# Kernel optimization log

Hardware: AMD Instinct MI355X
Metric: run time of the kernel (lower is better)

Reference implementation:

```python
import jax, jax.numpy as jnp
import numpy as np

N_NODES = 50000
N_EDGES = 800000
F_IN = 128
HIDDEN = 256
N_GRAPHS = 128


def setup_inputs() -> dict:
    key = jax.random.key(0)
    ks = jax.random.split(key, 13)
    x = jax.random.normal(ks[0], (N_NODES, F_IN), dtype=jnp.float32)
    edge_src = jax.random.randint(ks[1], (N_EDGES,), 0, N_NODES, dtype=jnp.int32)
    edge_dst = jax.random.randint(ks[2], (N_EDGES,), 0, N_NODES, dtype=jnp.int32)
    edge_w = jax.random.uniform(ks[3], (N_EDGES,), dtype=jnp.float32)
    seg_ids = jnp.sort(jax.random.randint(ks[4], (N_NODES,), 0, N_GRAPHS, dtype=jnp.int32))
    def lin(k, fan_in, fan_out):
        s = 1.0 / np.sqrt(fan_in)
        return jax.random.uniform(k, (fan_in, fan_out), dtype=jnp.float32, minval=-s, maxval=s)
    W1 = lin(ks[5], F_IN, HIDDEN);  b1 = jnp.zeros((HIDDEN,), jnp.float32)
    W2 = lin(ks[6], HIDDEN, HIDDEN); b2 = jnp.zeros((HIDDEN,), jnp.float32)
    Wd = lin(ks[7], HIDDEN, HIDDEN); bd = jnp.zeros((HIDDEN,), jnp.float32)
    Wo = lin(ks[8], HIDDEN, 1);      bo = jnp.zeros((1,), jnp.float32)
    return {"x": x, "edge_src": edge_src, "edge_dst": edge_dst, "edge_w": edge_w,
            "seg_ids": seg_ids, "W1": W1, "b1": b1, "W2": W2, "b2": b2,
            "Wd": Wd, "bd": bd, "Wo": Wo, "bo": bo}


def reference(x, edge_src, edge_dst, edge_w, seg_ids, W1, b1, W2, b2, Wd, bd, Wo, bo):
    n_nodes = x.shape[0]

    def spmm(h):
        # sparse A_norm @ h via gather-scale-scatter over the edge list
        msg = h[edge_src] * edge_w[:, None]            # [E, H]
        return jax.ops.segment_sum(msg, edge_dst, num_segments=n_nodes)

    # GCNConv 1: relu(A @ X @ W1 + b1); dropout p=0 is identity
    h = jax.nn.relu(spmm(x @ W1) + b1)                 # [N, H]
    # GCNConv 2
    h = jax.nn.relu(spmm(h @ W2) + b2)                 # [N, H]
    # GlobalSumPool keyed by graph index
    g = jax.ops.segment_sum(h, seg_ids, num_segments=N_GRAPHS)  # [G, H]
    # dense head
    g = jax.nn.relu(g @ Wd + bd)
    return g @ Wo + bo                                 # [G, 1]
```

## Files before the change

### kernel.cpp

```cpp
#include <hip/hip_runtime.h>
#include <hip/hip_bf16.h>


typedef short v8s __attribute__((ext_vector_type(8)));
typedef float v4f __attribute__((ext_vector_type(4)));
typedef float v2f __attribute__((ext_vector_type(2)));

#define BKT_CAP 6144

__device__ inline unsigned bf16u(float f) {
    unsigned u = __builtin_bit_cast(unsigned, f);
    return (u + 0x7fffu + ((u >> 16) & 1u)) >> 16;
}
__device__ inline float bflo(unsigned v) { return __builtin_bit_cast(float, v << 16); }
__device__ inline float bfhi(unsigned v) { return __builtin_bit_cast(float, v & 0xffff0000u); }

__global__ __launch_bounds__(256) void prep(
    const float* __restrict__ x, unsigned char* __restrict__ x8,
    const float* __restrict__ W1, ushort* __restrict__ Wt1,
    const float* __restrict__ W2, ushort* __restrict__ Wt2,
    int* __restrict__ bcnt)
{
    int b = blockIdx.x;
    int t = threadIdx.x;
    if (b < 6250) {
        int i = b * 256 + t;
        if (i < 1600000) {
            float4 v = ((const float4*)x)[i];
            int pk = __builtin_amdgcn_cvt_pk_fp8_f32(v.x, v.y, 0, false);
            pk = __builtin_amdgcn_cvt_pk_fp8_f32(v.z, v.w, pk, true);
            ((unsigned*)x8)[i] = (unsigned)pk;
        }
    } else if (b < 6506) {
        int n = b - 6250;
        if (t < 128) Wt1[n * 128 + t] = (ushort)bf16u(W1[t * 256 + n]);
    } else if (b < 6762) {
        int n = b - 6506;
        Wt2[n * 256 + t] = (ushort)bf16u(W2[t * 256 + n]);
    } else {
        bcnt[t] = 0;
    }
}

__global__ __launch_bounds__(256) void bin_pass(
    const int* __restrict__ src, const int* __restrict__ dst,
    const float* __restrict__ w, int* __restrict__ bcnt,
    uint2* __restrict__ stage, float* __restrict__ g, int E)
{
    __shared__ int hist[256];
    __shared__ int excl[256];
    __shared__ int gbase[256];
    __shared__ uint2 stg[2048];

    int t = threadIdx.x, b = blockIdx.x;
    if (b < 128) g[b * 256 + t] = 0.f;

    int e0 = b * 2048;
    hist[t] = 0;
    __syncthreads();

    int d_[8]; unsigned pk_[8]; int rk_[8]; int bk_[8];
    #pragma unroll
    for (int j = 0; j < 8; j++) {
        int e = e0 + t + j * 256;
        if (e < E) {
            int d = dst[e];
            d_[j] = d;
            bk_[j] = d >> 8;
            pk_[j] = (unsigned)src[e] | (bf16u(w[e]) << 16);
            rk_[j] = atomicAdd(&hist[bk_[j]], 1);
        } else d_[j] = -1;
    }
    __syncthreads();

    int cnt = hist[t];
    excl[t] = cnt;
    __syncthreads();
    for (int o = 1; o < 256; o <<= 1) {
        int v = (t >= o) ? excl[t - o] : 0;
        __syncthreads();
        excl[t] += v;
        __syncthreads();
    }
    int ex = excl[t] - cnt;
    if (cnt > 0) gbase[t] = atomicAdd(&bcnt[t], cnt);
    __syncthreads();
    excl[t] = ex;
    __syncthreads();

    #pragma unroll
    for (int j = 0; j < 8; j++)
        if (d_[j] >= 0)
            stg[excl[bk_[j]] + rk_[j]] = make_uint2(pk_[j], (unsigned)d_[j]);
    __syncthreads();

    int nval = min(2048, E - e0);
    #pragma unroll
    for (int j = 0; j < 8; j++) {
        int sidx = t + j * 256;
        if (sidx < nval) {
            uint2 ent = stg[sidx];
            int bk = (int)(ent.y >> 8);
            stage[(size_t)bk * BKT_CAP + gbase[bk] + sidx - excl[bk]] = ent;
        }
    }
}

__global__ __launch_bounds__(256) void sort_build(
    const uint2* __restrict__ stage, const int* __restrict__ bcnt,
    unsigned* __restrict__ edges, int* __restrict__ off, int N, int E)
{
    __shared__ unsigned sorted[BKT_CAP];
    __shared__ int hist[256];
    __shared__ int s[256];
    __shared__ int cur[256];
    __shared__ int psum[4];
    __shared__ int sbase;

    int t = threadIdx.x, b = blockIdx.x;
    const uint2* reg = stage + (size_t)b * BKT_CAP;
    int cnt = bcnt[b];

    int pred = (t < b) ? bcnt[t] : 0;
    #pragma unroll
    for (int o = 32; o > 0; o >>= 1) pred += __shfl_down(pred, o, 64);
    if ((t & 63) == 0) psum[t >> 6] = pred;
    hist[t] = 0;
    __syncthreads();
    if (t == 0) sbase = psum[0] + psum[1] + psum[2] + psum[3];

    for (int i = t; i < cnt; i += 256)
        atomicAdd(&hist[reg[i].y & 255u], 1);
    __syncthreads();

    int h = hist[t];
    s[t] = h;
    __syncthreads();
    for (int o = 1; o < 256; o <<= 1) {
        int v = (t >= o) ? s[t - o] : 0;
        __syncthreads();
        s[t] += v;
        __syncthreads();
    }
    int ex = s[t] - h;
    cur[t] = ex;
    __syncthreads();

    int nn = b * 256 + t;
    if (nn <= N) off[nn] = sbase + ex;

    for (int i = t; i < cnt; i += 256) {
        uint2 ent = reg[i];
        int r = atomicAdd(&cur[ent.y & 255u], 1);
        sorted[r] = ent.x;
    }
    __syncthreads();
    for (int i = t; i < cnt; i += 256)
        edges[sbase + i] = sorted[i];
}

__global__ __launch_bounds__(256) void spmm128(
    const unsigned char* __restrict__ x8, const int* __restrict__ off,
    const unsigned* __restrict__ edges, ushort* __restrict__ S, int n)
{
    int node = blockIdx.x * 4 + (threadIdx.x >> 6);
    if (node >= n) return;
    int lane = threadIdx.x & 63;
    const ushort* base = (const ushort*)x8;
    int e0 = off[node], e1 = off[node + 1];
    float a0 = 0.f, a1 = 0.f;
    int e = e0;
    for (; e + 16 <= e1; e += 16) {
        unsigned ed[16]; ushort v[16];
        #pragma unroll
        for (int j = 0; j < 16; j++) ed[j] = edges[e + j];
        #pragma unroll
        for (int j = 0; j < 16; j++)
            v[j] = base[(size_t)(ed[j] & 0xffffu) * 64 + lane];
        #pragma unroll
        for (int j = 0; j < 16; j++) {
            float w = bfhi(ed[j]);
            v2f f = __builtin_amdgcn_cvt_pk_f32_fp8((int)v[j], false);
            a0 += f.x * w;
            a1 += f.y * w;
        }
    }
    for (; e + 4 <= e1; e += 4) {
        unsigned ed[4]; ushort v[4];
        #pragma unroll
        for (int j = 0; j < 4; j++) ed[j] = edges[e + j];
        #pragma unroll
        for (int j = 0; j < 4; j++)
            v[j] = base[(size_t)(ed[j] & 0xffffu) * 64 + lane];
        #pragma unroll
        for (int j = 0; j < 4; j++) {
            float w = bfhi(ed[j]);
            v2f f = __builtin_amdgcn_cvt_pk_f32_fp8((int)v[j], false);
            a0 += f.x * w;
            a1 += f.y * w;
        }
    }
    for (; e < e1; e++) {
        unsigned ed = edges[e];
        float w0 = bfhi(ed);
        ushort v0 = base[(size_t)(ed & 0xffffu) * 64 + lane];
        v2f f0 = __builtin_amdgcn_cvt_pk_f32_fp8((int)v0, false);
        a0 += f0.x * w0;
        a1 += f0.y * w0;
    }
    ((unsigned*)S)[(size_t)node * 64 + lane] = (bf16u(a1) << 16) | bf16u(a0);
}

__global__ __launch_bounds__(256) void spmm256(
    const unsigned char* __restrict__ h8, const int* __restrict__ off,
    const unsigned* __restrict__ edges, ushort* __restrict__ S, int n)
{
    int node = blockIdx.x * 4 + (threadIdx.x >> 6);
    if (node >= n) return;
    int lane = threadIdx.x & 63;
    const unsigned* base = (const unsigned*)h8;
    int e0 = off[node], e1 = off[node + 1];
    float a0 = 0.f, a1 = 0.f, a2 = 0.f, a3 = 0.f;
    int e = e0;
    for (; e + 16 <= e1; e += 16) {
        unsigned ed[16]; unsigned v[16];
        #pragma unroll
        for (int j = 0; j < 16; j++) ed[j] = edges[e + j];
        #pragma unroll
        for (int j = 0; j < 16; j++)
            v[j] = base[(size_t)(ed[j] & 0xffffu) * 64 + lane];
        #pragma unroll
        for (int j = 0; j < 16; j++) {
            float w = bfhi(ed[j]);
            v2f l = __builtin_amdgcn_cvt_pk_f32_fp8((int)v[j], false);
            v2f h = __builtin_amdgcn_cvt_pk_f32_fp8((int)v[j], true);
            a0 += l.x * w;
            a1 += l.y * w;
            a2 += h.x * w;
            a3 += h.y * w;
        }
    }
    for (; e + 4 <= e1; e += 4) {
        unsigned ed[4]; unsigned v[4];
        #pragma unroll
        for (int j = 0; j < 4; j++) ed[j] = edges[e + j];
        #pragma unroll
        for (int j = 0; j < 4; j++)
            v[j] = base[(size_t)(ed[j] & 0xffffu) * 64 + lane];
        #pragma unroll
        for (int j = 0; j < 4; j++) {
            float w = bfhi(ed[j]);
            v2f l = __builtin_amdgcn_cvt_pk_f32_fp8((int)v[j], false);
            v2f h = __builtin_amdgcn_cvt_pk_f32_fp8((int)v[j], true);
            a0 += l.x * w;
            a1 += l.y * w;
            a2 += h.x * w;
            a3 += h.y * w;
        }
    }
    for (; e < e1; e++) {
        unsigned ed = edges[e];
        float w0 = bfhi(ed);
        unsigned v0 = base[(size_t)(ed & 0xffffu) * 64 + lane];
        v2f l0 = __builtin_amdgcn_cvt_pk_f32_fp8((int)v0, false);
        v2f h0 = __builtin_amdgcn_cvt_pk_f32_fp8((int)v0, true);
        a0 += l0.x * w0;
        a1 += l0.y * w0;
        a2 += h0.x * w0;
        a3 += h0.y * w0;
    }
    uint2 o;
    o.x = (bf16u(a1) << 16) | bf16u(a0);
    o.y = (bf16u(a3) << 16) | bf16u(a2);
    ((uint2*)S)[(size_t)node * 64 + lane] = o;
}

template <int K, int OFMT, bool POOL>
__global__ __launch_bounds__(512) void gemm_tile(
    const ushort* __restrict__ A, const ushort* __restrict__ Wt,
    const float* __restrict__ bias, void* __restrict__ out,
    const int* __restrict__ seg, float* __restrict__ g, int M)
{
    __shared__ __align__(16) ushort As[128 * 32];
    __shared__ __align__(16) ushort Bs[256 * 32];
    __shared__ int segsh[128];

    const int tid = threadIdx.x;
    const int bm = blockIdx.x * 128;
    const int wave = tid >> 6, lane = tid & 63;
    const int wm = wave >> 2, wn = wave & 3;
    const int r = lane & 15, q = lane >> 4;

    if (POOL && tid < 128) {
        int gr = bm + tid;
        segsh[tid] = (gr < M) ? seg[gr] : 0x7fffffff;
    }

    const int o0 = tid * 16;
    const int row0 = o0 >> 6;
    const int kb0 = o0 & 63;

    const char* Ab = (const char*)A;
    const char* Bb = (const char*)Wt;

    uint4 ra0, rb0, rb1;
    ra0 = *(const uint4*)(Ab + ((size_t)(bm + row0) * K) * 2 + kb0);
    rb0 = *(const uint4*)(Bb + ((size_t)(row0)       * K) * 2 + kb0);
    rb1 = *(const uint4*)(Bb + ((size_t)(row0 + 128) * K) * 2 + kb0);

    v4f acc[4][4];
    #pragma unroll
    for (int i = 0; i < 4; i++)
        #pragma unroll
        for (int j = 0; j < 4; j++) acc[i][j] = (v4f){0.f, 0.f, 0.f, 0.f};

    const int NK = K / 32;
    for (int ks = 0; ks < NK; ks++) {
        __syncthreads();
        *(uint4*)((char*)As + o0)        = ra0;
        *(uint4*)((char*)Bs + o0)        = rb0;
        *(uint4*)((char*)Bs + o0 + 8192) = rb1;
        if (ks + 1 < NK) {
            const int kof = (ks + 1) * 64;
            ra0 = *(const uint4*)(Ab + ((size_t)(bm + row0) * K) * 2 + kof + kb0);
            rb0 = *(const uint4*)(Bb + ((size_t)(row0)       * K) * 2 + kof + kb0);
            rb1 = *(const uint4*)(Bb + ((size_t)(row0 + 128) * K) * 2 + kof + kb0);
        }
        __syncthreads();

        v8s af[4], bf[4];
        #pragma unroll
        for (int i = 0; i < 4; i++)
            af[i] = *(const v8s*)(As + (wm * 64 + i * 16 + r) * 32 + q * 8);
        #pragma unroll
        for (int j = 0; j < 4; j++)
            bf[j] = *(const v8s*)(Bs + (wn * 64 + j * 16 + r) * 32 + q * 8);
        #pragma unroll
        for (int i = 0; i < 4; i++)
            #pragma unroll
            for (int j = 0; j < 4; j++)
                acc[i][j] = __builtin_amdgcn_mfma_f32_16x16x32_bf16(
                    af[i], bf[j], acc[i][j], 0, 0, 0);
    }

    if constexpr (POOL) {
        #pragma unroll
        for (int j = 0; j < 4; j++) {
            float b = bias[wn * 64 + j * 16 + r];
            #pragma unroll
            for (int i = 0; i < 4; i++)
                #pragma unroll
                for (int ii = 0; ii < 4; ii++)
                    acc[i][j][ii] = fmaxf(acc[i][j][ii] + b, 0.f);
        }
        int myseg[16];
        #pragma unroll
        for (int i = 0; i < 4; i++)
            #pragma unroll
            for (int ii = 0; ii < 4; ii++)
                myseg[i * 4 + ii] = segsh[wm * 64 + i * 16 + q * 4 + ii];
        int s_lo = segsh[0];
        int s_hi = segsh[min(127, M - 1 - bm)];
        for (int s = s_lo; s <= s_hi; s++) {
            #pragma unroll
            for (int j = 0; j < 4; j++) {
                float p = 0.f;
                #pragma unroll
                for (int i = 0; i < 4; i++)
                    #pragma unroll
                    for (int ii = 0; ii < 4; ii++)
                        if (myseg[i * 4 + ii] == s) p += acc[i][j][ii];
                p += __shfl_xor(p, 16, 64);
                p += __shfl_xor(p, 32, 64);
                if (lane < 16)
                    atomicAdd(&g[s * 256 + wn * 64 + j * 16 + r], p);
            }
        }
    } else {
        #pragma unroll
        for (int j = 0; j < 4; j++) {
            int col = wn * 64 + j * 16 + r;
            float b = bias[col];
            #pragma unroll
            for (int i = 0; i < 4; i++) {
                #pragma unroll
                for (int ii = 0; ii < 4; ii++) {
                    int row = bm + wm * 64 + i * 16 + q * 4 + ii;
                    if (row < M) {
                        float v = fmaxf(acc[i][j][ii] + b, 0.f);
                        if constexpr (OFMT == 1) {
                            ((ushort*)out)[(size_t)row * 256 + col] = (ushort)bf16u(v);
                        } else if constexpr (OFMT == 2) {
                            unsigned pk = (unsigned)__builtin_amdgcn_cvt_pk_fp8_f32(
                                v, v, 0, false);
                            ((unsigned char*)out)[(size_t)row * 256 + col] =
                                (unsigned char)(pk & 0xffu);
                        } else {
                            ((float*)out)[(size_t)row * 256 + col] = v;
                        }
                    }
                }
            }
        }
    }
}

__global__ __launch_bounds__(256) void head(
    const float* __restrict__ g, const float* __restrict__ Wd,
    const float* __restrict__ bd, const float* __restrict__ Wo,
    const float* __restrict__ bo, float* __restrict__ out)
{
    __shared__ float gr[256];
    int j = threadIdx.x;
    int gi = blockIdx.x;
    gr[j] = g[(size_t)gi * 256 + j];
    __syncthreads();
    float a2 = bd[j];
    for (int k = 0; k < 256; k++)
        a2 += gr[k] * Wd[(size_t)k * 256 + j];
    a2 = fmaxf(a2, 0.f);

    float v = a2 * Wo[j];
    #pragma unroll
    for (int off = 32; off > 0; off >>= 1)
        v += __shfl_down(v, off, 64);
    __shared__ float partial[4];
    if ((j & 63) == 0) partial[j >> 6] = v;
    __syncthreads();
    if (j == 0)
        out[gi] = partial[0] + partial[1] + partial[2] + partial[3] + bo[0];
}

extern "C" void kernel_launch(void* const* d_in, const int* in_sizes, int n_in,
                              void* d_out, int out_size, void* d_ws, size_t ws_size,
                              hipStream_t stream) {
    const float* x   = (const float*)d_in[0];
    const int*   esrc= (const int*)  d_in[1];
    const int*   edst= (const int*)  d_in[2];
    const float* ew  = (const float*)d_in[3];
    const int*   seg = (const int*)  d_in[4];
    const float* W1  = (const float*)d_in[5];
    const float* b1  = (const float*)d_in[6];
    const float* W2  = (const float*)d_in[7];
    const float* b2  = (const float*)d_in[8];
    const float* Wd  = (const float*)d_in[9];
    const float* bd  = (const float*)d_in[10];
    const float* Wo  = (const float*)d_in[11];
    const float* bo  = (const float*)d_in[12];
    float* out = (float*)d_out;

    const int N = 50000, E = 800000, G = 128, H = 256, F = 128;
    const int NPAD = 50048;
    const int NB = (N + 255) / 256;

    char* p = (char*)d_ws;
    char* region0 = p;                  p += (size_t)N * H * sizeof(float);
    unsigned char* x8 = (unsigned char*)region0;
    ushort* S1 = (ushort*)(region0 + (size_t)N * F);
    uint2* stage = (uint2*)(region0 + (size_t)32 * 1024 * 1024);
    unsigned char* h8 = (unsigned char*)p;
                                        p += (size_t)N * H;
    ushort* S2 = (ushort*)p;            p += (size_t)NPAD * H * sizeof(ushort);
    float* g   = (float*)p;             p += (size_t)G * H * sizeof(float);
    int*   bcnt= (int*)p;               p += 256 * sizeof(int);
    int*   off = (int*)p;               p += (size_t)(N + 1) * sizeof(int) + 12;
    unsigned* edges=(unsigned*)p;       p += (size_t)E * sizeof(unsigned);
    ushort* Wt1= (ushort*)p;            p += (size_t)H * F * sizeof(ushort);
    ushort* Wt2= (ushort*)p;            p += (size_t)H * H * sizeof(ushort);

    prep<<<6763, 256, 0, stream>>>(x, x8, W1, Wt1, W2, Wt2, bcnt);
    bin_pass<<<(E + 2047) / 2048, 256, 0, stream>>>(esrc, edst, ew, bcnt, stage, g, E);
    sort_build<<<NB, 256, 0, stream>>>(stage, bcnt, edges, off, N, E);

    spmm128<<<(N + 3) / 4, 256, 0, stream>>>(x8, off, edges, S1, N);
    gemm_tile<128, 2, false><<<NPAD / 128, 512, 0, stream>>>(
        S1, Wt1, b1, h8, nullptr, nullptr, N);

    spmm256<<<(N + 3) / 4, 256, 0, stream>>>(h8, off, edges, S2, N);
    gemm_tile<256, 0, true><<<NPAD / 128, 512, 0, stream>>>(
        S2, Wt2, b2, nullptr, seg, g, N);

    head<<<G, 256, 0, stream>>>(g, Wd, bd, Wo, bo, out);
}
```

Before: 227.0 us.

## Fuse SpMM aggregation with dense GEMM per 64-node tile in shared memory

Measured after the change: 251.6 us. +10.9%, slower.

```diff
diff --git a/kernel.cpp b/kernel.cpp
--- a/kernel.cpp
+++ b/kernel.cpp
@@ -159,184 +159,167 @@
         edges[sbase + i] = sorted[i];
 }
 
-__global__ __launch_bounds__(256) void spmm128(
-    const unsigned char* __restrict__ x8, const int* __restrict__ off,
-    const unsigned* __restrict__ edges, ushort* __restrict__ S, int n)
-{
-    int node = blockIdx.x * 4 + (threadIdx.x >> 6);
-    if (node >= n) return;
-    int lane = threadIdx.x & 63;
-    const ushort* base = (const ushort*)x8;
-    int e0 = off[node], e1 = off[node + 1];
-    float a0 = 0.f, a1 = 0.f;
-    int e = e0;
-    for (; e + 16 <= e1; e += 16) {
-        unsigned ed[16]; ushort v[16];
-        #pragma unroll
-        for (int j = 0; j < 16; j++) ed[j] = edges[e + j];
-        #pragma unroll
-        for (int j = 0; j < 16; j++)
-            v[j] = base[(size_t)(ed[j] & 0xffffu) * 64 + lane];
-        #pragma unroll
-        for (int j = 0; j < 16; j++) {
-            float w = bfhi(ed[j]);
-            v2f f = __builtin_amdgcn_cvt_pk_f32_fp8((int)v[j], false);
-            a0 += f.x * w;
-            a1 += f.y * w;
-        }
-    }
-    for (; e + 4 <= e1; e += 4) {
-        unsigned ed[4]; ushort v[4];
-        #pragma unroll
-        for (int j = 0; j < 4; j++) ed[j] = edges[e + j];
-        #pragma unroll
-        for (int j = 0; j < 4; j++)
-            v[j] = base[(size_t)(ed[j] & 0xffffu) * 64 + lane];
-        #pragma unroll
-        for (int j = 0; j < 4; j++) {
-            float w = bfhi(ed[j]);
-            v2f f = __builtin_amdgcn_cvt_pk_f32_fp8((int)v[j], false);
-            a0 += f.x * w;
-            a1 += f.y * w;
-        }
-    }
-    for (; e < e1; e++) {
-        unsigned ed = edges[e];
-        float w0 = bfhi(ed);
-        ushort v0 = base[(size_t)(ed & 0xffffu) * 64 + lane];
-        v2f f0 = __builtin_amdgcn_cvt_pk_f32_fp8((int)v0, false);
-        a0 += f0.x * w0;
-        a1 += f0.y * w0;
-    }
-    ((unsigned*)S)[(size_t)node * 64 + lane] = (bf16u(a1) << 16) | bf16u(a0);
-}
-
-__global__ __launch_bounds__(256) void spmm256(
-    const unsigned char* __restrict__ h8, const int* __restrict__ off,
-    const unsigned* __restrict__ edges, ushort* __restrict__ S, int n)
-{
-    int node = blockIdx.x * 4 + (threadIdx.x >> 6);
-    if (node >= n) return;
-    int lane = threadIdx.x & 63;
-    const unsigned* base = (const unsigned*)h8;
-    int e0 = off[node], e1 = off[node + 1];
-    float a0 = 0.f, a1 = 0.f, a2 = 0.f, a3 = 0.f;
-    int e = e0;
-    for (; e + 16 <= e1; e += 16) {
-        unsigned ed[16]; unsigned v[16];
-        #pragma unroll
-        for (int j = 0; j < 16; j++) ed[j] = edges[e + j];
-        #pragma unroll
-        for (int j = 0; j < 16; j++)
-            v[j] = base[(size_t)(ed[j] & 0xffffu) * 64 + lane];
-        #pragma unroll
-        for (int j = 0; j < 16; j++) {
-            float w = bfhi(ed[j]);
-            v2f l = __builtin_amdgcn_cvt_pk_f32_fp8((int)v[j], false);
-            v2f h = __builtin_amdgcn_cvt_pk_f32_fp8((int)v[j], true);
-            a0 += l.x * w;
-            a1 += l.y * w;
-            a2 += h.x * w;
-            a3 += h.y * w;
-        }
-    }
-    for (; e + 4 <= e1; e += 4) {
-        unsigned ed[4]; unsigned v[4];
-        #pragma unroll
-        for (int j = 0; j < 4; j++) ed[j] = edges[e + j];
-        #pragma unroll
-        for (int j = 0; j < 4; j++)
-            v[j] = base[(size_t)(ed[j] & 0xffffu) * 64 + lane];
-        #pragma unroll
-        for (int j = 0; j < 4; j++) {
-            float w = bfhi(ed[j]);
-            v2f l = __builtin_amdgcn_cvt_pk_f32_fp8((int)v[j], false);
-            v2f h = __builtin_amdgcn_cvt_pk_f32_fp8((int)v[j], true);
-            a0 += l.x * w;
-            a1 += l.y * w;
-            a2 += h.x * w;
-            a3 += h.y * w;
-        }
-    }
-    for (; e < e1; e++) {
-        unsigned ed = edges[e];
-        float w0 = bfhi(ed);
-        unsigned v0 = base[(size_t)(ed & 0xffffu) * 64 + lane];
-        v2f l0 = __builtin_amdgcn_cvt_pk_f32_fp8((int)v0, false);
-        v2f h0 = __builtin_amdgcn_cvt_pk_f32_fp8((int)v0, true);
-        a0 += l0.x * w0;
-        a1 += l0.y * w0;
-        a2 += h0.x * w0;
-        a3 += h0.y * w0;
-    }
-    uint2 o;
-    o.x = (bf16u(a1) << 16) | bf16u(a0);
-    o.y = (bf16u(a3) << 16) | bf16u(a2);
-    ((uint2*)S)[(size_t)node * 64 + lane] = o;
-}
-
-template <int K, int OFMT, bool POOL>
-__global__ __launch_bounds__(512) void gemm_tile(
-    const ushort* __restrict__ A, const ushort* __restrict__ Wt,
+template <int KIN, int OFMT, bool POOL>
+__global__ __launch_bounds__(512) void fused_layer(
+    const unsigned char* __restrict__ feat, const int* __restrict__ off,
+    const unsigned* __restrict__ edges, const ushort* __restrict__ Wt,
     const float* __restrict__ bias, void* __restrict__ out,
     const int* __restrict__ seg, float* __restrict__ g, int M)
 {
-    __shared__ __align__(16) ushort As[128 * 32];
+    constexpr int AST = KIN + 8;
+    __shared__ __align__(16) ushort At[64 * AST];
     __shared__ __align__(16) ushort Bs[256 * 32];
-    __shared__ int segsh[128];
+    __shared__ int segsh[64];
 
     const int tid = threadIdx.x;
-    const int bm = blockIdx.x * 128;
+    const int bm = blockIdx.x * 64;
     const int wave = tid >> 6, lane = tid & 63;
+
+    if (POOL && tid < 64) {
+        int gr = bm + tid;
+        segsh[tid] = (gr < M) ? seg[gr] : 0x7fffffff;
+    }
+
+    for (int i = 0; i < 8; i++) {
+        int nl = wave * 8 + i;
+        int node = bm + nl;
+        if (node < M) {
+            int e0 = off[node], e1 = off[node + 1];
+            if (KIN == 256) {
+                const unsigned* base = (const unsigned*)feat;
+                float a0 = 0.f, a1 = 0.f, a2 = 0.f, a3 = 0.f;
+                int e = e0;
+                for (; e + 16 <= e1; e += 16) {
+                    unsigned ed[16]; unsigned v[16];
+                    #pragma unroll
+                    for (int j = 0; j < 16; j++) ed[j] = edges[e + j];
+                    #pragma unroll
+                    for (int j = 0; j < 16; j++)
+                        v[j] = base[(size_t)(ed[j] & 0xffffu) * 64 + lane];
+                    #pragma unroll
+                    for (int j = 0; j < 16; j++) {
+                        float w = bfhi(ed[j]);
+                        v2f l = __builtin_amdgcn_cvt_pk_f32_fp8((int)v[j], false);
+                        v2f h = __builtin_amdgcn_cvt_pk_f32_fp8((int)v[j], true);
+                        a0 += l.x * w; a1 += l.y * w;
+                        a2 += h.x * w; a3 += h.y * w;
+                    }
+                }
+                for (; e + 4 <= e1; e += 4) {
+                    unsigned ed[4]; unsigned v[4];
+                    #pragma unroll
+                    for (int j = 0; j < 4; j++) ed[j] = edges[e + j];
+                    #pragma unroll
+                    for (int j = 0; j < 4; j++)
+                        v[j] = base[(size_t)(ed[j] & 0xffffu) * 64 + lane];
+                    #pragma unroll
+                    for (int j = 0; j < 4; j++) {
+                        float w = bfhi(ed[j]);
+                        v2f l = __builtin_amdgcn_cvt_pk_f32_fp8((int)v[j], false);
+                        v2f h = __builtin_amdgcn_cvt_pk_f32_fp8((int)v[j], true);
+                        a0 += l.x * w; a1 += l.y * w;
+                        a2 += h.x * w; a3 += h.y * w;
+                    }
+                }
+                for (; e < e1; e++) {
+                    unsigned ed = edges[e];
+                    float w0 = bfhi(ed);
+                    unsigned v0 = base[(size_t)(ed & 0xffffu) * 64 + lane];
+                    v2f l0 = __builtin_amdgcn_cvt_pk_f32_fp8((int)v0, false);
+                    v2f h0 = __builtin_amdgcn_cvt_pk_f32_fp8((int)v0, true);
+                    a0 += l0.x * w0; a1 += l0.y * w0;
+                    a2 += h0.x * w0; a3 += h0.y * w0;
+                }
+                uint2 o;
+                o.x = (bf16u(a1) << 16) | bf16u(a0);
+                o.y = (bf16u(a3) << 16) | bf16u(a2);
+                *(uint2*)(At + nl * AST + lane * 4) = o;
+            } else {
+                const ushort* base = (const ushort*)feat;
+                float a0 = 0.f, a1 = 0.f;
+                int e = e0;
+                for (; e + 16 <= e1; e += 16) {
+                    unsigned ed[16]; ushort v[16];
+                    #pragma unroll
+                    for (int j = 0; j < 16; j++) ed[j] = edges[e + j];
+                    #pragma unroll
+                    for (int j = 0; j < 16; j++)
+                        v[j] = base[(size_t)(ed[j] & 0xffffu) * 64 + lane];
+                    #pragma unroll
+                    for (int j = 0; j < 16; j++) {
+                        float w = bfhi(ed[j]);
+                        v2f f = __builtin_amdgcn_cvt_pk_f32_fp8((int)v[j], false);
+                        a0 += f.x * w; a1 += f.y * w;
+                    }
+                }
+                for (; e + 4 <= e1; e += 4) {
+                    unsigned ed[4]; ushort v[4];
+                    #pragma unroll
+                    for (int j = 0; j < 4; j++) ed[j] = edges[e + j];
+                    #pragma unroll
+                    for (int j = 0; j < 4; j++)
+                        v[j] = base[(size_t)(ed[j] & 0xffffu) * 64 + lane];
+                    #pragma unroll
+                    for (int j = 0; j < 4; j++) {
+                        float w = bfhi(ed[j]);
+                        v2f f = __builtin_amdgcn_cvt_pk_f32_fp8((int)v[j], false);
+                        a0 += f.x * w; a1 += f.y * w;
+                    }
+                }
+                for (; e < e1; e++) {
+                    unsigned ed = edges[e];
+                    float w0 = bfhi(ed);
+                    ushort v0 = base[(size_t)(ed & 0xffffu) * 64 + lane];
+                    v2f f0 = __builtin_amdgcn_cvt_pk_f32_fp8((int)v0, false);
+                    a0 += f0.x * w0; a1 += f0.y * w0;
+                }
+                *(unsigned*)(At + nl * AST + lane * 2) =
+                    (bf16u(a1) << 16) | bf16u(a0);
+            }
+        } else {
+            if (KIN == 256) *(uint2*)(At + nl * AST + lane * 4) = make_uint2(0u, 0u);
+            else            *(unsigned*)(At + nl * AST + lane * 2) = 0u;
+        }
+    }
+
     const int wm = wave >> 2, wn = wave & 3;
     const int r = lane & 15, q = lane >> 4;
-
-    if (POOL && tid < 128) {
-        int gr = bm + tid;
-        segsh[tid] = (gr < M) ? seg[gr] : 0x7fffffff;
-    }
 
     const int o0 = tid * 16;
     const int row0 = o0 >> 6;
     const int kb0 = o0 & 63;
-
-    const char* Ab = (const char*)A;
     const char* Bb = (const char*)Wt;
 
-    uint4 ra0, rb0, rb1;
-    ra0 = *(const uint4*)(Ab + ((size_t)(bm + row0) * K) * 2 + kb0);
-    rb0 = *(const uint4*)(Bb + ((size_t)(row0)       * K) * 2 + kb0);
-    rb1 = *(const uint4*)(Bb + ((size_t)(row0 + 128) * K) * 2 + kb0);
-
-    v4f acc[4][4];
-    #pragma unroll
-    for (int i = 0; i < 4; i++)
+    uint4 rb0 = *(const uint4*)(Bb + ((size_t)(row0)       * KIN) * 2 + kb0);
+    uint4 rb1 = *(const uint4*)(Bb + ((size_t)(row0 + 128) * KIN) * 2 + kb0);
+
+    v4f acc[2][4];
+    #pragma unroll
+    for (int i = 0; i < 2; i++)
         #pragma unroll
         for (int j = 0; j < 4; j++) acc[i][j] = (v4f){0.f, 0.f, 0.f, 0.f};
 
-    const int NK = K / 32;
+    const int NK = KIN / 32;
     for (int ks = 0; ks < NK; ks++) {
         __syncthreads();
-        *(uint4*)((char*)As + o0)        = ra0;
         *(uint4*)((char*)Bs + o0)        = rb0;
         *(uint4*)((char*)Bs + o0 + 8192) = rb1;
         if (ks + 1 < NK) {
             const int kof = (ks + 1) * 64;
-            ra0 = *(const uint4*)(Ab + ((size_t)(bm + row0) * K) * 2 + kof + kb0);
-            rb0 = *(const uint4*)(Bb + ((size_t)(row0)       * K) * 2 + kof + kb0);
-            rb1 = *(const uint4*)(Bb + ((size_t)(row0 + 128) * K) * 2 + kof + kb0);
-        }
-        __syncthreads();
-
-        v8s af[4], bf[4];
-        #pragma unroll
-        for (int i = 0; i < 4; i++)
-            af[i] = *(const v8s*)(As + (wm * 64 + i * 16 + r) * 32 + q * 8);
+            rb0 = *(const uint4*)(Bb + ((size_t)(row0)       * KIN) * 2 + kof + kb0);
+            rb1 = *(const uint4*)(Bb + ((size_t)(row0 + 128) * KIN) * 2 + kof + kb0);
+        }
+        __syncthreads();
+
+        v8s af[2], bf[4];
+        #pragma unroll
+        for (int i = 0; i < 2; i++)
+            af[i] = *(const v8s*)(At + (wm * 32 + i * 16 + r) * AST + ks * 32 + q * 8);
         #pragma unroll
         for (int j = 0; j < 4; j++)
             bf[j] = *(const v8s*)(Bs + (wn * 64 + j * 16 + r) * 32 + q * 8);
         #pragma unroll
-        for (int i = 0; i < 4; i++)
+        for (int i = 0; i < 2; i++)
             #pragma unroll
             for (int j = 0; j < 4; j++)
                 acc[i][j] = __builtin_amdgcn_mfma_f32_16x16x32_bf16(
@@ -348,25 +331,25 @@
         for (int j = 0; j < 4; j++) {
             float b = bias[wn * 64 + j * 16 + r];
             #pragma unroll
-            for (int i = 0; i < 4; i++)
+            for (int i = 0; i < 2; i++)
                 #pragma unroll
                 for (int ii = 0; ii < 4; ii++)
                     acc[i][j][ii] = fmaxf(acc[i][j][ii] + b, 0.f);
         }
-        int myseg[16];
-        #pragma unroll
-        for (int i = 0; i < 4; i++)
+        int myseg[8];
+        #pragma unroll
+        for (int i = 0; i < 2; i++)
             #pragma unroll
             for (int ii = 0; ii < 4; ii++)
-                myseg[i * 4 + ii] = segsh[wm * 64 + i * 16 + q * 4 + ii];
+                myseg[i * 4 + ii] = segsh[wm * 32 + i * 16 + q * 4 + ii];
         int s_lo = segsh[0];
-        int s_hi = segsh[min(127, M - 1 - bm)];
+        int s_hi = segsh[min(63, M - 1 - bm)];
         for (int s = s_lo; s <= s_hi; s++) {
             #pragma unroll
             for (int j = 0; j < 4; j++) {
                 float p = 0.f;
                 #pragma unroll
-                for (int i = 0; i < 4; i++)
+                for (int i = 0; i < 2; i++)
                     #pragma unroll
                     for (int ii = 0; ii < 4; ii++)
                         if (myseg[i * 4 + ii] == s) p += acc[i][j][ii];
@@ -382,21 +365,19 @@
             int col = wn * 64 + j * 16 + r;
             float b = bias[col];
             #pragma unroll
-            for (int i = 0; i < 4; i++) {
+            for (int i = 0; i < 2; i++) {
                 #pragma unroll
                 for (int ii = 0; ii < 4; ii++) {
-                    int row = bm + wm * 64 + i * 16 + q * 4 + ii;
+                    int row = bm + wm * 32 + i * 16 + q * 4 + ii;
                     if (row < M) {
                         float v = fmaxf(acc[i][j][ii] + b, 0.f);
-                        if constexpr (OFMT == 1) {
-                            ((ushort*)out)[(size_t)row * 256 + col] = (ushort)bf16u(v);
-                        } else if constexpr (OFMT == 2) {
+                        if constexpr (OFMT == 2) {
                             unsigned pk = (unsigned)__builtin_amdgcn_cvt_pk_fp8_f32(
                                 v, v, 0, false);
                             ((unsigned char*)out)[(size_t)row * 256 + col] =
                                 (unsigned char)(pk & 0xffu);
                         } else {
-                            ((float*)out)[(size_t)row * 256 + col] = v;
+                            ((ushort*)out)[(size_t)row * 256 + col] = (ushort)bf16u(v);
                         }
                     }
                 }
@@ -450,17 +431,15 @@
     float* out = (float*)d_out;
 
     const int N = 50000, E = 800000, G = 128, H = 256, F = 128;
-    const int NPAD = 50048;
     const int NB = (N + 255) / 256;
+    const int NBLK = (N + 63) / 64;
 
     char* p = (char*)d_ws;
     char* region0 = p;                  p += (size_t)N * H * sizeof(float);
     unsigned char* x8 = (unsigned char*)region0;
-    ushort* S1 = (ushort*)(region0 + (size_t)N * F);
     uint2* stage = (uint2*)(region0 + (size_t)32 * 1024 * 1024);
     unsigned char* h8 = (unsigned char*)p;
                                         p += (size_t)N * H;
-    ushort* S2 = (ushort*)p;            p += (size_t)NPAD * H * sizeof(ushort);
     float* g   = (float*)p;             p += (size_t)G * H * sizeof(float);
     int*   bcnt= (int*)p;               p += 256 * sizeof(int);
     int*   off = (int*)p;               p += (size_t)(N + 1) * sizeof(int) + 12;
@@ -472,13 +451,11 @@
     bin_pass<<<(E + 2047) / 2048, 256, 0, stream>>>(esrc, edst, ew, bcnt, stage, g, E);
     sort_build<<<NB, 256, 0, stream>>>(stage, bcnt, edges, off, N, E);
 
-    spmm128<<<(N + 3) / 4, 256, 0, stream>>>(x8, off, edges, S1, N);
-    gemm_tile<128, 2, false><<<NPAD / 128, 512, 0, stream>>>(
-        S1, Wt1, b1, h8, nullptr, nullptr, N);
-
-    spmm256<<<(N + 3) / 4, 256, 0, stream>>>(h8, off, edges, S2, N);
-    gemm_tile<256, 0, true><<<NPAD / 128, 512, 0, stream>>>(
-        S2, Wt2, b2, nullptr, seg, g, N);
+    fused_layer<128, 2, false><<<NBLK, 512, 0, stream>>>(
+        x8, off, edges, Wt1, b1, h8, nullptr, nullptr, N);
+
+    fused_layer<256, 0, true><<<NBLK, 512, 0, stream>>>(
+        h8, off, edges, Wt2, b2, nullptr, seg, g, N);
 
     head<<<G, 256, 0, stream>>>(g, Wd, bd, Wo, bo, out);
 }
```
